# Kernel tuning notes

Hardware: AMD Instinct MI355X
Metric: run time of the kernel (lower is better)

Reference implementation:

```python
import jax, jax.numpy as jnp
import numpy as np

B, S, HID = 2, 4096, 2048
H, D, R = 4, 64, 32  # num_index_heads, head_dim, rope_head_dim
LN_EPS = 1e-5


def rotate_half(x):
    x1, x2 = jnp.split(x, 2, axis=-1)
    return jnp.concatenate([-x2, x1], axis=-1)


def setup_inputs() -> dict:
    key = jax.random.key(0)
    ks = jax.random.split(key, 8)
    hidden_states = jax.random.normal(ks[0], (B, S, HID), jnp.float32)
    cos = jax.random.uniform(ks[1], (B, S, R), jnp.float32)
    sin = jax.random.uniform(ks[2], (B, S, R), jnp.float32)
    Wq = jax.random.normal(ks[3], (HID, H * D), jnp.float32) * 0.02
    Wk = jax.random.normal(ks[4], (HID, D), jnp.float32) * 0.02
    Ww = jax.random.normal(ks[5], (HID, H), jnp.float32) * 0.02
    ln_gamma = jnp.ones((D,), jnp.float32)
    ln_beta = jnp.zeros((D,), jnp.float32)
    return {"hidden_states": hidden_states, "cos": cos, "sin": sin,
            "Wq": Wq, "Wk": Wk, "Ww": Ww,
            "ln_gamma": ln_gamma, "ln_beta": ln_beta}


def reference(hidden_states, cos, sin, Wq, Wk, Ww, ln_gamma, ln_beta):
    b, s, _ = hidden_states.shape
    h = Ww.shape[1]
    d = Wk.shape[1]
    r = cos.shape[-1]

    # projections
    q = (hidden_states @ Wq).reshape(b, s, h, d)      # [B,S,H,D]
    k = hidden_states @ Wk                             # [B,S,D]
    w = hidden_states @ Ww                             # [B,S,H]

    # LayerNorm on k over head_dim
    mu = jnp.mean(k, axis=-1, keepdims=True)
    var = jnp.mean(jnp.square(k - mu), axis=-1, keepdims=True)
    k = (k - mu) * jax.lax.rsqrt(var + LN_EPS) * ln_gamma + ln_beta

    # partial RoPE on first r dims
    q_pe, q_nope = q[..., :r], q[..., r:]
    k_pe, k_nope = k[..., :r], k[..., r:]
    cos_q = cos[:, :, None, :]
    sin_q = sin[:, :, None, :]
    q_pe = q_pe * cos_q + rotate_half(q_pe) * sin_q
    k_pe = k_pe * cos + rotate_half(k_pe) * sin
    q = jnp.concatenate([q_pe, q_nope], axis=-1)       # [B,S,H,D]
    k = jnp.concatenate([k_pe, k_nope], axis=-1)       # [B,S,D]

    # relu(q k^T), single shared key head broadcast over index heads
    score = jax.nn.relu(jnp.einsum('bqhd,bkd->bhqk', q, k))  # [B,H,Sq,Sk]
    # per-query, per-head weights, summed over heads
    indexer_score = jnp.einsum('bqh,bhqk->bqk', w, score)    # [B,Sq,Sk]
    return indexer_score
```

## Files before the change

### kernel.cpp

```cpp
#include <hip/hip_runtime.h>

#define BDIM 2
#define SDIM 4096
#define HIDDEN 2048
#define NH 4
#define DD 64
#define RR 32
constexpr float LN_EPS = 1e-5f;

typedef _Float16 half8 __attribute__((ext_vector_type(8)));
typedef __attribute__((ext_vector_type(4))) float f32x4;

__device__ __forceinline__ void gload_lds16(const void* g, void* l) {
    __builtin_amdgcn_global_load_lds(
        (const __attribute__((address_space(1))) void*)g,
        (__attribute__((address_space(3))) void*)l, 16, 0, 0);
}

__global__ __launch_bounds__(256) void split_hs(
    const float* __restrict__ hs, _Float16* __restrict__ hs2)
{
    const int idx  = blockIdx.x * 256 + threadIdx.x;
    const int m    = idx >> 8;
    const int slot = idx & 255;
    const float4 v0 = *reinterpret_cast<const float4*>(&hs[(size_t)m * HIDDEN + slot * 8]);
    const float4 v1 = *reinterpret_cast<const float4*>(&hs[(size_t)m * HIDDEN + slot * 8 + 4]);
    _Float16 o[8];
    o[0] = (_Float16)v0.x; o[1] = (_Float16)v0.y;
    o[2] = (_Float16)v0.z; o[3] = (_Float16)v0.w;
    o[4] = (_Float16)v1.x; o[5] = (_Float16)v1.y;
    o[6] = (_Float16)v1.z; o[7] = (_Float16)v1.w;
    const int eoff = (slot * 8) ^ ((m & 7) << 3);
    *reinterpret_cast<half8*>(&hs2[(size_t)m * HIDDEN + eoff]) =
        *reinterpret_cast<half8*>(o);
}

__global__ __launch_bounds__(256) void prep_w2(
    const float* __restrict__ Wq, const float* __restrict__ Wk,
    const float* __restrict__ Ww, _Float16* __restrict__ Wt2)
{
    __shared__ float T[64][65];
    const int k0 = blockIdx.x * 64, n0 = blockIdx.y * 64;
    const int tid = threadIdx.x;
    {
        const int kr = tid >> 2;
        const int nq = (tid & 3) * 16;
        const int gk = k0 + kr;
        #pragma unroll
        for (int c = 0; c < 16; ++c) {
            const int n = n0 + nq + c;
            float v;
            if (n < 256)      v = Wq[(size_t)gk * 256 + n];
            else if (n < 320) v = Wk[(size_t)gk * 64 + (n - 256)];
            else if (n < 324) v = Ww[(size_t)gk * NH + (n - 320)];
            else              v = 0.f;
            T[kr][nq + c] = v;
        }
    }
    __syncthreads();
    {
        const int nr = tid >> 2;
        const int kc = (tid & 3) * 16;
        const int n  = n0 + nr;
        #pragma unroll
        for (int s = 0; s < 2; ++s) {
            const int kb = kc + s * 8;
            _Float16 e[8];
            #pragma unroll
            for (int t = 0; t < 8; ++t) e[t] = (_Float16)T[kb + t][nr];
            const int eoff = (k0 + kb) ^ ((nr & 7) << 3);
            *reinterpret_cast<half8*>(&Wt2[(size_t)n * HIDDEN + eoff]) =
                *reinterpret_cast<half8*>(e);
        }
    }
}

__global__ __launch_bounds__(256) void proj_mfma(
    const _Float16* __restrict__ hs2, const _Float16* __restrict__ Wt2,
    const float* __restrict__ cosb, const float* __restrict__ sinb,
    const float* __restrict__ gamma, const float* __restrict__ beta,
    _Float16* __restrict__ qout, _Float16* __restrict__ kout,
    float* __restrict__ wout)
{
    __shared__ _Float16 Asm[128 * 128];
    __shared__ _Float16 Bsm[64 * 128];

    const int m0   = blockIdx.x * 128;
    const int ng   = blockIdx.y;
    const int tid  = threadIdx.x;
    const int wave = tid >> 6, lane = tid & 63;
    const int lr = lane & 15, lh = lane >> 4;

    f32x4 acc[2][4];
    #pragma unroll
    for (int i = 0; i < 2; ++i)
        #pragma unroll
        for (int j = 0; j < 4; ++j)
            acc[i][j] = (f32x4){0.f, 0.f, 0.f, 0.f};

    const int srow  = tid >> 4;
    const int sslot = tid & 15;
    const _Float16* gA = hs2 + (size_t)(m0 + srow) * HIDDEN + sslot * 8;
    const _Float16* gB = Wt2 + (size_t)(ng * 64 + srow) * HIDDEN + sslot * 8;
    _Float16* lA = Asm + tid * 8;
    _Float16* lB = Bsm + tid * 8;

    for (int k0 = 0; k0 < HIDDEN; k0 += 128) {
        #pragma unroll
        for (int i = 0; i < 8; ++i)
            gload_lds16(gA + (size_t)i * 16 * HIDDEN + k0, lA + i * 2048);
        #pragma unroll
        for (int i = 0; i < 4; ++i)
            gload_lds16(gB + (size_t)i * 16 * HIDDEN + k0, lB + i * 2048);
        __syncthreads();

        #pragma unroll
        for (int kk = 0; kk < 4; ++kk) {
            half8 av[2], bv[4];
            #pragma unroll
            for (int i = 0; i < 2; ++i) {
                const int row = wave * 32 + i * 16 + lr;
                const int off = (row * 128 + kk * 32 + lh * 8) ^ ((row & 7) << 3);
                av[i] = *reinterpret_cast<const half8*>(&Asm[off]);
            }
            #pragma unroll
            for (int j = 0; j < 4; ++j) {
                const int row = j * 16 + lr;
                const int off = (row * 128 + kk * 32 + lh * 8) ^ ((row & 7) << 3);
                bv[j] = *reinterpret_cast<const half8*>(&Bsm[off]);
            }
            #pragma unroll
            for (int i = 0; i < 2; ++i)
                #pragma unroll
                for (int j = 0; j < 4; ++j)
                    acc[i][j] = __builtin_amdgcn_mfma_f32_16x16x32_f16(
                        av[i], bv[j], acc[i][j], 0, 0, 0);
        }
        __syncthreads();
    }

    if (ng < 4) {
        #pragma unroll
        for (int i = 0; i < 2; ++i)
            #pragma unroll
            for (int r = 0; r < 4; ++r) {
                const int m = m0 + wave * 32 + i * 16 + lh * 4 + r;
                const float x0 = acc[i][0][r], x1 = acc[i][1][r];
                const float c0 = cosb[(size_t)m * RR + lr];
                const float s0 = sinb[(size_t)m * RR + lr];
                const float c1 = cosb[(size_t)m * RR + 16 + lr];
                const float s1 = sinb[(size_t)m * RR + 16 + lr];
                const int sw = (m & 7) << 3;
                const size_t rowb = (size_t)m * (NH * DD);
                const int e0 = ng * DD + lr;
                qout[rowb + (e0 ^ sw)]        = (_Float16)(x0 * c0 - x1 * s0);
                qout[rowb + ((e0 + 16) ^ sw)] = (_Float16)(x1 * c1 + x0 * s1);
                qout[rowb + ((e0 + 32) ^ sw)] = (_Float16)acc[i][2][r];
                qout[rowb + ((e0 + 48) ^ sw)] = (_Float16)acc[i][3][r];
            }
    } else if (ng == 4) {
        float g[4], bb[4];
        #pragma unroll
        for (int j = 0; j < 4; ++j) { g[j] = gamma[j * 16 + lr]; bb[j] = beta[j * 16 + lr]; }
        #pragma unroll
        for (int i = 0; i < 2; ++i)
            #pragma unroll
            for (int r = 0; r < 4; ++r) {
                float t1 = 0.f, t2 = 0.f;
                #pragma unroll
                for (int j = 0; j < 4; ++j) {
                    const float a = acc[i][j][r];
                    t1 += a; t2 += a * a;
                }
                #pragma unroll
                for (int msk = 1; msk < 16; msk <<= 1) {
                    t1 += __shfl_xor(t1, msk, 64);
                    t2 += __shfl_xor(t2, msk, 64);
                }
                const float mu  = t1 * (1.f / 64.f);
                const float var = t2 * (1.f / 64.f) - mu * mu;
                const float rs  = rsqrtf(var + LN_EPS);
                const int m = m0 + wave * 32 + i * 16 + lh * 4 + r;
                float x[4];
                #pragma unroll
                for (int j = 0; j < 4; ++j)
                    x[j] = (acc[i][j][r] - mu) * rs * g[j] + bb[j];
                const float c0 = cosb[(size_t)m * RR + lr];
                const float s0 = sinb[(size_t)m * RR + lr];
                const float c1 = cosb[(size_t)m * RR + 16 + lr];
                const float s1 = sinb[(size_t)m * RR + 16 + lr];
                const float y0 = x[0] * c0 - x[1] * s0;
                const float y1 = x[1] * c1 + x[0] * s1;
                const size_t base = (size_t)m * DD + lr;
                kout[base]      = (_Float16)y0;
                kout[base + 16] = (_Float16)y1;
                kout[base + 32] = (_Float16)x[2];
                kout[base + 48] = (_Float16)x[3];
            }
    } else {
        if (lr < NH) {
            #pragma unroll
            for (int i = 0; i < 2; ++i)
                #pragma unroll
                for (int r = 0; r < 4; ++r) {
                    const int m = m0 + wave * 32 + i * 16 + lh * 4 + r;
                    wout[(size_t)m * NH + lr] = acc[i][0][r];
                }
        }
    }
}

__global__ __launch_bounds__(256) void score_kernel(
    const _Float16* __restrict__ qb, const _Float16* __restrict__ kb,
    const float* __restrict__ wr, float* __restrict__ out)
{
    __shared__ _Float16 Qlds[64 * 256];
    __shared__ float Wlds[64 * 4];

    const int kc  = blockIdx.x;
    const int q0  = blockIdx.y * 64;
    const int b   = blockIdx.z;
    const int tid = threadIdx.x;
    const int wave = tid >> 6, lane = tid & 63;
    const int wm = wave >> 1, wn = wave & 1;
    const int lr = lane & 15, lh = lane >> 4;
    const int kbase = kc * 512;

    #pragma unroll
    for (int i = 0; i < 8; ++i) {
        const int id = i * 256 + tid;
        gload_lds16(qb + (size_t)(b * SDIM + q0 + (id >> 5)) * 256 + (id & 31) * 8,
                    Qlds + id * 8);
    }
    Wlds[tid] = wr[(size_t)(b * SDIM + q0) * NH + tid];

    const size_t krow_base = (size_t)(b * SDIM + kbase + wn * 32);
    #define LOADK(dst, st)                                                      \
        _Pragma("unroll")                                                       \
        for (int j = 0; j < 2; ++j)                                             \
            _Pragma("unroll")                                                   \
            for (int ks = 0; ks < 2; ++ks)                                      \
                dst[j][ks] = *reinterpret_cast<const half8*>(                   \
                    &kb[(krow_base + (st) * 64 + j * 16 + lr) * DD + ks * 32 + lh * 8]);

    half8 kcur[2][2], knx[2][2];
    LOADK(kcur, 0)

    __syncthreads();

    f32x4 wreg[2][4];
    #pragma unroll
    for (int i = 0; i < 2; ++i)
        #pragma unroll
        for (int r = 0; r < 4; ++r)
            wreg[i][r] = *reinterpret_cast<const f32x4*>(
                &Wlds[(wm * 32 + i * 16 + lh * 4 + r) * 4]);

    for (int st = 0; st < 8; ++st) {
        if (st < 7) { LOADK(knx, st + 1) }

        f32x4 o[2][2];
        #pragma unroll
        for (int i = 0; i < 2; ++i)
            #pragma unroll
            for (int j = 0; j < 2; ++j)
                o[i][j] = (f32x4){0.f, 0.f, 0.f, 0.f};

        #pragma unroll
        for (int h = 0; h < NH; ++h) {
            half8 qf[2][2];
            #pragma unroll
            for (int i = 0; i < 2; ++i)
                #pragma unroll
                for (int ks = 0; ks < 2; ++ks) {
                    const int row  = wm * 32 + i * 16 + lr;
                    const int slot = (h * 8 + ks * 4 + lh) ^ (row & 7);
                    qf[i][ks] = *reinterpret_cast<const half8*>(
                        &Qlds[row * 256 + slot * 8]);
                }
            f32x4 s[2][2];
            #pragma unroll
            for (int i = 0; i < 2; ++i)
                #pragma unroll
                for (int j = 0; j < 2; ++j)
                    s[i][j] = (f32x4){0.f, 0.f, 0.f, 0.f};
            __builtin_amdgcn_s_setprio(1);
            #pragma unroll
            for (int ks = 0; ks < 2; ++ks)
                #pragma unroll
                for (int i = 0; i < 2; ++i)
                    #pragma unroll
                    for (int j = 0; j < 2; ++j)
                        s[i][j] = __builtin_amdgcn_mfma_f32_16x16x32_f16(
                            qf[i][ks], kcur[j][ks], s[i][j], 0, 0, 0);
            __builtin_amdgcn_s_setprio(0);
            #pragma unroll
            for (int i = 0; i < 2; ++i)
                #pragma unroll
                for (int j = 0; j < 2; ++j)
                    #pragma unroll
                    for (int r = 0; r < 4; ++r)
                        o[i][j][r] += wreg[i][r][h] * fmaxf(s[i][j][r], 0.f);
        }

        #pragma unroll
        for (int i = 0; i < 2; ++i)
            #pragma unroll
            for (int r = 0; r < 4; ++r)
                #pragma unroll
                for (int j = 0; j < 2; ++j)
                    out[(size_t)(b * SDIM + q0 + wm * 32 + i * 16 + lh * 4 + r) * SDIM
                        + kbase + st * 64 + wn * 32 + j * 16 + lr] = o[i][j][r];

        #pragma unroll
        for (int j = 0; j < 2; ++j)
            #pragma unroll
            for (int ks = 0; ks < 2; ++ks)
                kcur[j][ks] = knx[j][ks];
    }
    #undef LOADK
}

extern "C" void kernel_launch(void* const* d_in, const int* in_sizes, int n_in,
                              void* d_out, int out_size, void* d_ws, size_t ws_size,
                              hipStream_t stream) {
    const float* hs    = (const float*)d_in[0];
    const float* cosb  = (const float*)d_in[1];
    const float* sinb  = (const float*)d_in[2];
    const float* Wq    = (const float*)d_in[3];
    const float* Wk    = (const float*)d_in[4];
    const float* Ww    = (const float*)d_in[5];
    const float* gamma = (const float*)d_in[6];
    const float* beta  = (const float*)d_in[7];
    float* out = (float*)d_out;

    _Float16* hs2 = (_Float16*)d_out;

    char* wsb = (char*)d_ws;
    _Float16* qb  = (_Float16*)wsb;
    _Float16* kb  = (_Float16*)(wsb + (size_t)BDIM * SDIM * 256 * 2);
    float*    ww  = (float*)(wsb + (size_t)BDIM * SDIM * 256 * 2
                                  + (size_t)BDIM * SDIM * DD * 2);
    _Float16* Wt2 = (_Float16*)(wsb + (size_t)BDIM * SDIM * 256 * 2
                                     + (size_t)BDIM * SDIM * DD * 2
                                     + (size_t)BDIM * SDIM * NH * 4);

    prep_w2<<<dim3(HIDDEN / 64, 6), 256, 0, stream>>>(Wq, Wk, Ww, Wt2);

    split_hs<<<(BDIM * SDIM * (HIDDEN / 8)) / 256, 256, 0, stream>>>(hs, hs2);

    proj_mfma<<<dim3((BDIM * SDIM) / 128, 6), 256, 0, stream>>>(
        hs2, Wt2, cosb, sinb, gamma, beta, qb, kb, ww);

    score_kernel<<<dim3(SDIM / 512, SDIM / 64, BDIM), 256, 0, stream>>>(
        qb, kb, ww, out);
}
```

Before: 85.18 us.

## Fuse fp32-to-fp16 hidden-state conversion into projection GEMM register loads

Removes the separate split_hs kernel that converted hidden states to a swizzled fp16 buffer. The projection kernel now loads fp32 hidden states straight from global memory into registers, converts them to fp16 there, and feeds the MFMA A operand without LDS staging. This saves a full write and re-read of the 32MB-scale converted buffer plus one kernel launch. In exchange, each of the 6 column-group blocks rereads the fp32 A rows, doubling the bytes per A load, and the per-lane strided global loads are less coalesced than the LDS path.

```diff
diff --git a/kernel.cpp b/kernel.cpp
--- a/kernel.cpp
+++ b/kernel.cpp
@@ -15,24 +15,6 @@
     __builtin_amdgcn_global_load_lds(
         (const __attribute__((address_space(1))) void*)g,
         (__attribute__((address_space(3))) void*)l, 16, 0, 0);
-}
-
-__global__ __launch_bounds__(256) void split_hs(
-    const float* __restrict__ hs, _Float16* __restrict__ hs2)
-{
-    const int idx  = blockIdx.x * 256 + threadIdx.x;
-    const int m    = idx >> 8;
-    const int slot = idx & 255;
-    const float4 v0 = *reinterpret_cast<const float4*>(&hs[(size_t)m * HIDDEN + slot * 8]);
-    const float4 v1 = *reinterpret_cast<const float4*>(&hs[(size_t)m * HIDDEN + slot * 8 + 4]);
-    _Float16 o[8];
-    o[0] = (_Float16)v0.x; o[1] = (_Float16)v0.y;
-    o[2] = (_Float16)v0.z; o[3] = (_Float16)v0.w;
-    o[4] = (_Float16)v1.x; o[5] = (_Float16)v1.y;
-    o[6] = (_Float16)v1.z; o[7] = (_Float16)v1.w;
-    const int eoff = (slot * 8) ^ ((m & 7) << 3);
-    *reinterpret_cast<half8*>(&hs2[(size_t)m * HIDDEN + eoff]) =
-        *reinterpret_cast<half8*>(o);
 }
 
 __global__ __launch_bounds__(256) void prep_w2(
@@ -76,13 +58,12 @@
 }
 
 __global__ __launch_bounds__(256) void proj_mfma(
-    const _Float16* __restrict__ hs2, const _Float16* __restrict__ Wt2,
+    const float* __restrict__ hs, const _Float16* __restrict__ Wt2,
     const float* __restrict__ cosb, const float* __restrict__ sinb,
     const float* __restrict__ gamma, const float* __restrict__ beta,
     _Float16* __restrict__ qout, _Float16* __restrict__ kout,
     float* __restrict__ wout)
 {
-    __shared__ _Float16 Asm[128 * 128];
     __shared__ _Float16 Bsm[64 * 128];
 
     const int m0   = blockIdx.x * 128;
@@ -100,29 +81,36 @@
 
     const int srow  = tid >> 4;
     const int sslot = tid & 15;
-    const _Float16* gA = hs2 + (size_t)(m0 + srow) * HIDDEN + sslot * 8;
     const _Float16* gB = Wt2 + (size_t)(ng * 64 + srow) * HIDDEN + sslot * 8;
-    _Float16* lA = Asm + tid * 8;
     _Float16* lB = Bsm + tid * 8;
 
+    const float* gA = hs + (size_t)(m0 + wave * 32 + lr) * HIDDEN + lh * 8;
+
     for (int k0 = 0; k0 < HIDDEN; k0 += 128) {
-        #pragma unroll
-        for (int i = 0; i < 8; ++i)
-            gload_lds16(gA + (size_t)i * 16 * HIDDEN + k0, lA + i * 2048);
         #pragma unroll
         for (int i = 0; i < 4; ++i)
             gload_lds16(gB + (size_t)i * 16 * HIDDEN + k0, lB + i * 2048);
+
+        half8 av[2][4];
+        #pragma unroll
+        for (int i = 0; i < 2; ++i)
+            #pragma unroll
+            for (int kk = 0; kk < 4; ++kk) {
+                const float* p = gA + (size_t)i * 16 * HIDDEN + k0 + kk * 32;
+                const float4 a = *reinterpret_cast<const float4*>(p);
+                const float4 b = *reinterpret_cast<const float4*>(p + 4);
+                half8 h;
+                h[0] = (_Float16)a.x; h[1] = (_Float16)a.y;
+                h[2] = (_Float16)a.z; h[3] = (_Float16)a.w;
+                h[4] = (_Float16)b.x; h[5] = (_Float16)b.y;
+                h[6] = (_Float16)b.z; h[7] = (_Float16)b.w;
+                av[i][kk] = h;
+            }
         __syncthreads();
 
         #pragma unroll
         for (int kk = 0; kk < 4; ++kk) {
-            half8 av[2], bv[4];
-            #pragma unroll
-            for (int i = 0; i < 2; ++i) {
-                const int row = wave * 32 + i * 16 + lr;
-                const int off = (row * 128 + kk * 32 + lh * 8) ^ ((row & 7) << 3);
-                av[i] = *reinterpret_cast<const half8*>(&Asm[off]);
-            }
+            half8 bv[4];
             #pragma unroll
             for (int j = 0; j < 4; ++j) {
                 const int row = j * 16 + lr;
@@ -134,7 +122,7 @@
                 #pragma unroll
                 for (int j = 0; j < 4; ++j)
                     acc[i][j] = __builtin_amdgcn_mfma_f32_16x16x32_f16(
-                        av[i], bv[j], acc[i][j], 0, 0, 0);
+                        av[i][kk], bv[j], acc[i][j], 0, 0, 0);
         }
         __syncthreads();
     }
@@ -334,8 +322,6 @@
     const float* beta  = (const float*)d_in[7];
     float* out = (float*)d_out;
 
-    _Float16* hs2 = (_Float16*)d_out;
-
     char* wsb = (char*)d_ws;
     _Float16* qb  = (_Float16*)wsb;
     _Float16* kb  = (_Float16*)(wsb + (size_t)BDIM * SDIM * 256 * 2);
@@ -347,10 +333,8 @@
 
     prep_w2<<<dim3(HIDDEN / 64, 6), 256, 0, stream>>>(Wq, Wk, Ww, Wt2);
 
-    split_hs<<<(BDIM * SDIM * (HIDDEN / 8)) / 256, 256, 0, stream>>>(hs, hs2);
-
     proj_mfma<<<dim3((BDIM * SDIM) / 128, 6), 256, 0, stream>>>(
-        hs2, Wt2, cosb, sinb, gamma, beta, qb, kb, ww);
+        hs, Wt2, cosb, sinb, gamma, beta, qb, kb, ww);
 
     score_kernel<<<dim3(SDIM / 512, SDIM / 64, BDIM), 256, 0, stream>>>(
         qb, kb, ww, out);
```

Measured after the change: 112.4 us. 32.0% more time.

## Merge prep kernels and permute k rows for vectorized float2 output stores

Applied to the files above, without the earlier changes.

Fuses the weight-transpose and hidden-state fp16 conversion kernels into one launch, dispatching on block index, which removes one kernel launch. Permutes the row order of the k buffer within each 32-token group so that each lane's two score columns become adjacent, letting the score kernel write its output as float2 stores instead of scalar stores. The output is the dominant memory traffic, so wider stores target store efficiency. This relies on the score kernel's k loading matching the new interleaved layout.

```diff
diff --git a/kernel.cpp b/kernel.cpp
--- a/kernel.cpp
+++ b/kernel.cpp
@@ -17,31 +17,34 @@
         (__attribute__((address_space(3))) void*)l, 16, 0, 0);
 }
 
-__global__ __launch_bounds__(256) void split_hs(
-    const float* __restrict__ hs, _Float16* __restrict__ hs2)
-{
-    const int idx  = blockIdx.x * 256 + threadIdx.x;
-    const int m    = idx >> 8;
-    const int slot = idx & 255;
-    const float4 v0 = *reinterpret_cast<const float4*>(&hs[(size_t)m * HIDDEN + slot * 8]);
-    const float4 v1 = *reinterpret_cast<const float4*>(&hs[(size_t)m * HIDDEN + slot * 8 + 4]);
-    _Float16 o[8];
-    o[0] = (_Float16)v0.x; o[1] = (_Float16)v0.y;
-    o[2] = (_Float16)v0.z; o[3] = (_Float16)v0.w;
-    o[4] = (_Float16)v1.x; o[5] = (_Float16)v1.y;
-    o[6] = (_Float16)v1.z; o[7] = (_Float16)v1.w;
-    const int eoff = (slot * 8) ^ ((m & 7) << 3);
-    *reinterpret_cast<half8*>(&hs2[(size_t)m * HIDDEN + eoff]) =
-        *reinterpret_cast<half8*>(o);
-}
-
-__global__ __launch_bounds__(256) void prep_w2(
+__global__ __launch_bounds__(256) void prep_split(
+    const float* __restrict__ hs, _Float16* __restrict__ hs2,
     const float* __restrict__ Wq, const float* __restrict__ Wk,
     const float* __restrict__ Ww, _Float16* __restrict__ Wt2)
 {
     __shared__ float T[64][65];
-    const int k0 = blockIdx.x * 64, n0 = blockIdx.y * 64;
     const int tid = threadIdx.x;
+
+    if (blockIdx.x < 8192) {
+        const int idx  = blockIdx.x * 256 + tid;
+        const int m    = idx >> 8;
+        const int slot = idx & 255;
+        const float4 v0 = *reinterpret_cast<const float4*>(&hs[(size_t)m * HIDDEN + slot * 8]);
+        const float4 v1 = *reinterpret_cast<const float4*>(&hs[(size_t)m * HIDDEN + slot * 8 + 4]);
+        _Float16 o[8];
+        o[0] = (_Float16)v0.x; o[1] = (_Float16)v0.y;
+        o[2] = (_Float16)v0.z; o[3] = (_Float16)v0.w;
+        o[4] = (_Float16)v1.x; o[5] = (_Float16)v1.y;
+        o[6] = (_Float16)v1.z; o[7] = (_Float16)v1.w;
+        const int eoff = (slot * 8) ^ ((m & 7) << 3);
+        *reinterpret_cast<half8*>(&hs2[(size_t)m * HIDDEN + eoff]) =
+            *reinterpret_cast<half8*>(o);
+        return;
+    }
+
+    const int pb = blockIdx.x - 8192;
+    const int k0 = (pb & 31) * 64;
+    const int n0 = (pb >> 5) * 64;
     {
         const int kr = tid >> 2;
         const int nq = (tid & 3) * 16;
@@ -191,7 +194,9 @@
                 const float s1 = sinb[(size_t)m * RR + 16 + lr];
                 const float y0 = x[0] * c0 - x[1] * s0;
                 const float y1 = x[1] * c1 + x[0] * s1;
-                const size_t base = (size_t)m * DD + lr;
+                const int tok  = m & 31;
+                const int prow = (m & ~31) | ((tok & 1) << 4) | (tok >> 1);
+                const size_t base = (size_t)prow * DD + lr;
                 kout[base]      = (_Float16)y0;
                 kout[base + 16] = (_Float16)y1;
                 kout[base + 32] = (_Float16)x[2];
@@ -306,11 +311,13 @@
         #pragma unroll
         for (int i = 0; i < 2; ++i)
             #pragma unroll
-            for (int r = 0; r < 4; ++r)
-                #pragma unroll
-                for (int j = 0; j < 2; ++j)
-                    out[(size_t)(b * SDIM + q0 + wm * 32 + i * 16 + lh * 4 + r) * SDIM
-                        + kbase + st * 64 + wn * 32 + j * 16 + lr] = o[i][j][r];
+            for (int r = 0; r < 4; ++r) {
+                float2 v;
+                v.x = o[i][0][r]; v.y = o[i][1][r];
+                *reinterpret_cast<float2*>(
+                    &out[(size_t)(b * SDIM + q0 + wm * 32 + i * 16 + lh * 4 + r) * SDIM
+                        + kbase + st * 64 + wn * 32 + 2 * lr]) = v;
+            }
 
         #pragma unroll
         for (int j = 0; j < 2; ++j)
@@ -345,9 +352,7 @@
                                      + (size_t)BDIM * SDIM * DD * 2
                                      + (size_t)BDIM * SDIM * NH * 4);
 
-    prep_w2<<<dim3(HIDDEN / 64, 6), 256, 0, stream>>>(Wq, Wk, Ww, Wt2);
-
-    split_hs<<<(BDIM * SDIM * (HIDDEN / 8)) / 256, 256, 0, stream>>>(hs, hs2);
+    prep_split<<<8192 + 192, 256, 0, stream>>>(hs, hs2, Wq, Wk, Ww, Wt2);
 
     proj_mfma<<<dim3((BDIM * SDIM) / 128, 6), 256, 0, stream>>>(
         hs2, Wt2, cosb, sinb, gamma, beta, qb, kb, ww);
```

After: 94.95 us. 1.11x slower.
